# Optimization experiments

Hardware: AMD Instinct MI355X
Metric: run time of the kernel (lower is better)

The kernel has to match this reference:

```python
import jax, jax.numpy as jnp
import numpy as np

B, N0, NCLS = 8, 1024, 40
SPACING, SIGMA_FACTOR = 2.0, 1.0
BLOCKS = [[64, 64], [128, 128], [256, 1024]]
POOL_SIZES = [256, 64, 1]
FC1, FC2 = 512, 256
# 3x3x3 kernel translation grid (27-point support, hard-coded in ConvLayer)
GRID = jnp.asarray(np.array([[i, j, k] for i in (-1, 0, 1) for j in (-1, 0, 1) for k in (-1, 0, 1)], dtype=np.float32))  # [27,3]


def pcnn_conv(pc, feat, W, b, sigma):
    """Extension-operator point convolution.
    pc [B,N,3], feat [B,N,Cin], W [27,Cin,Cout], b [Cout].
    out[b,i,o] = relu( (1/N) * sum_l sum_j exp(-||p_i - p_j + t_l||^2/(2 ks^2)) f[b,j] @ W[l] + b )
    """
    ks = SIGMA_FACTOR * sigma
    trans = SPACING * sigma * GRID                      # [27,3]
    inv = 1.0 / (2.0 * ks * ks)
    diff = pc[:, :, None, :] - pc[:, None, :, :]        # [B,N,N,3]
    d2 = jnp.sum(diff * diff, -1)                       # [B,N,N]
    n = pc.shape[1]

    def body(acc, wt):
        t, Wl = wt                                      # t [3], Wl [Cin,Cout]
        # ||diff + t||^2 = d2 + 2 diff.t + |t|^2
        e = jnp.exp(-(d2 + 2.0 * jnp.einsum('bijd,d->bij', diff, t) + jnp.dot(t, t)) * inv)
        s = jnp.einsum('bij,bjc->bic', e, feat)         # Gaussian-weighted gather
        return acc + jnp.einsum('bic,co->bio', s, Wl), None

    out0 = jnp.zeros((pc.shape[0], n, W.shape[2]), feat.dtype)
    out, _ = jax.lax.scan(body, out0, (trans, W))
    return jax.nn.relu(out / n + b)


def fps(pts, m):
    """Farthest point sampling. pts [N,3] -> indices [m]."""
    d = jnp.sum((pts - pts[0]) ** 2, -1)
    idxs = jnp.zeros((m,), jnp.int32)

    def body(i, state):
        idxs, d = state
        nxt = jnp.argmax(d).astype(jnp.int32)
        idxs = idxs.at[i].set(nxt)
        d = jnp.minimum(d, jnp.sum((pts - pts[nxt]) ** 2, -1))
        return idxs, d

    idxs, _ = jax.lax.fori_loop(1, m, body, (idxs, d))
    return idxs


def pool(pc, feat, m):
    """FPS subsample to m centers, max-pool features over nearest-center clusters."""
    idx = jax.vmap(lambda p: fps(p, m))(pc)                      # [B,m]
    centers = jnp.take_along_axis(pc, idx[..., None], axis=1)    # [B,m,3]
    dist = jnp.sum((pc[:, :, None, :] - centers[:, None, :, :]) ** 2, -1)  # [B,N,m]
    assign = jnp.argmin(dist, -1)                                # [B,N]
    pooled = jax.vmap(lambda f, a: jax.ops.segment_max(f, a, num_segments=m))(feat, assign)
    return centers, pooled


def bn(x, g, b):
    mu = jnp.mean(x, 0)
    v = jnp.var(x, 0)
    return g * (x - mu) * jax.lax.rsqrt(v + 1e-5) + b


def setup_inputs() -> dict:
    key = jax.random.key(0)
    ks = jax.random.split(key, 24)
    inp = {"pc": jax.random.normal(ks[0], (B, 3, N0), jnp.float32)}
    chans = [4, 64, 64, 128, 128, 256, 1024]
    for i, (ci, co) in enumerate(zip(chans[:-1], chans[1:])):
        inp[f"w_c{i}"] = jax.random.normal(ks[1 + i], (27, ci, co), jnp.float32) * 0.05
        inp[f"b_c{i}"] = jnp.zeros((co,), jnp.float32)
    inp["w_fc1"] = jax.random.normal(ks[10], (1024, FC1), jnp.float32) * 0.03
    inp["g_fc1"] = jnp.ones((FC1,), jnp.float32)
    inp["be_fc1"] = jnp.zeros((FC1,), jnp.float32)
    inp["w_fc2"] = jax.random.normal(ks[11], (FC1, FC2), jnp.float32) * 0.05
    inp["g_fc2"] = jnp.ones((FC2,), jnp.float32)
    inp["be_fc2"] = jnp.zeros((FC2,), jnp.float32)
    inp["w_fc3"] = jax.random.normal(ks[12], (FC2, NCLS), jnp.float32) * 0.05
    inp["b_fc3"] = jnp.zeros((NCLS,), jnp.float32)
    return inp


def reference(pc, w_c0, b_c0, w_c1, b_c1, w_c2, b_c2, w_c3, b_c3, w_c4, b_c4, w_c5, b_c5,
              w_fc1, g_fc1, be_fc1, w_fc2, g_fc2, be_fc2, w_fc3, b_fc3):
    pts = jnp.transpose(pc, (0, 2, 1))                           # [B,N,3]
    b_, n0, _ = pts.shape
    feat = jnp.concatenate([pts, jnp.ones((b_, n0, 1), pts.dtype)], -1)  # [B,N,4]
    sigma = 1.0 / float(np.sqrt(n0))  # faithfully uses initial N for all blocks
    ws = [(w_c0, b_c0), (w_c1, b_c1), (w_c2, b_c2), (w_c3, b_c3), (w_c4, b_c4), (w_c5, b_c5)]
    idx = 0
    cur = pts
    for bi, block in enumerate(BLOCKS):
        for _ in block:
            W, bb = ws[idx]
            feat = pcnn_conv(cur, feat, W, bb, sigma)
            idx += 1
        cur, feat = pool(cur, feat, POOL_SIZES[bi])
    x = feat.reshape(b_, -1)                                     # [B,1024]
    x = jax.nn.relu(bn(x @ w_fc1, g_fc1, be_fc1))
    x = jax.nn.relu(bn(x @ w_fc2, g_fc2, be_fc2))
    return x @ w_fc3 + b_fc3
```

## Files before the change

### kernel.cpp

```cpp
#include <hip/hip_runtime.h>
#include <cstdint>
#include <cstddef>
#include <cmath>

constexpr int B = 8;
constexpr int N0 = 1024;
constexpr int CAP = 64;
using u16 = unsigned short;

typedef __bf16 bf16x8 __attribute__((ext_vector_type(8)));
typedef float f32x4 __attribute__((ext_vector_type(4)));

__device__ inline u16 f2bf(float x) {
  unsigned u = __float_as_uint(x);
  return (u16)((u + 0x7fffu + ((u >> 16) & 1u)) >> 16);
}
__device__ inline float bf2f(u16 h) { return __uint_as_float(((unsigned)h) << 16); }
__device__ inline int swk2(int row, int k) {
  int s = (((row >> 2) ^ (row >> 4)) & 3);
  return ((((k >> 3) ^ s) << 3) | (k & 7));
}

__global__ __launch_bounds__(256) void k_prep(const float* __restrict__ pc,
                                              float* __restrict__ pts,
                                              float* __restrict__ feat0,
                                              uint4* __restrict__ p3, int n3,
                                              uint4* __restrict__ p6, int n6,
                                              uint4* __restrict__ p9, int n9) {
  int idx = blockIdx.x * blockDim.x + threadIdx.x;
  if (idx < B * N0) {
    int b = idx / N0, i = idx - b * N0;
    float x = pc[(b * 3 + 0) * N0 + i];
    float y = pc[(b * 3 + 1) * N0 + i];
    float z = pc[(b * 3 + 2) * N0 + i];
    pts[idx * 3 + 0] = x; pts[idx * 3 + 1] = y; pts[idx * 3 + 2] = z;
    feat0[idx * 4 + 0] = x; feat0[idx * 4 + 1] = y; feat0[idx * 4 + 2] = z; feat0[idx * 4 + 3] = 1.0f;
  }
  uint4 v = make_uint4(0xFFFFFFFFu, 0xFFFFFFFFu, 0xFFFFFFFFu, 0xFFFFFFFFu);
  for (int i = idx; i < n3; i += B * N0) p3[i] = v;
  for (int i = idx; i < n6; i += B * N0) p6[i] = v;
  for (int i = idx; i < n9; i += B * N0) p9[i] = v;
}

__global__ __launch_bounds__(256) void k_pairs(const float* __restrict__ pts,
                                               int* __restrict__ pidx, int* __restrict__ pcnt,
                                               int N) {
  const int r = blockIdx.x * 4 + (threadIdx.x >> 6);
  const int lane = threadIdx.x & 63;
  const int b = r / N;
  const float px = pts[(size_t)r * 3 + 0];
  const float py = pts[(size_t)r * 3 + 1];
  const float pz = pts[(size_t)r * 3 + 2];
  int* row = pidx + (size_t)r * CAP;
  int base = 0;
  for (int j0 = 0; j0 < N; j0 += 64) {
    int j = j0 + lane;
    float dx = px - pts[((size_t)b * N + j) * 3 + 0];
    float dy = py - pts[((size_t)b * N + j) * 3 + 1];
    float dz = pz - pts[((size_t)b * N + j) * 3 + 2];
    float d2 = dx * dx + dy * dy + dz * dz;
    bool keep = d2 <= 0.1228f;
    unsigned long long mk = __ballot(keep);
    int pos = __popcll(mk & ((1ull << lane) - 1ull));
    if (keep) { int s = base + pos; if (s < CAP) row[s] = j; }
    base += __popcll(mk);
  }
  if (lane == 0) pcnt[r] = base < CAP ? base : CAP;
}

__device__ __forceinline__ void econ_dev(float (*eL)[28],
                                         const float* __restrict__ pts,
                                         const float* __restrict__ feat,
                                         const int* __restrict__ pidx,
                                         const int* __restrict__ pcnt,
                                         u16* __restrict__ Shi, u16* __restrict__ Slo,
                                         int N, int Cin, int K, int Kpad, int mbase,
                                         int blockX) {
  const int g = mbase + blockX;
  const int b = g / N;
  const int t = threadIdx.x;
  const int w = t >> 6, lane = t & 63;
  const bool cact = t < Cin;
  const float px = pts[(size_t)g * 3 + 0];
  const float py = pts[(size_t)g * 3 + 1];
  const float pz = pts[(size_t)g * 3 + 2];
  float sxc = 0.f, syc = 0.f, szc = 0.f, cst = 0.f;
  if (lane < 27) {
    int a = lane / 9, bb = (lane / 3) % 3, cc = lane % 3;
    sxc = (a == 0) ? 64.f : ((a == 2) ? -64.f : 0.f);
    syc = (bb == 0) ? 64.f : ((bb == 2) ? -64.f : 0.f);
    szc = (cc == 0) ? 64.f : ((cc == 2) ? -64.f : 0.f);
    cst = -2.f * (float)((a != 1) + (bb != 1) + (cc != 1));
  }
  float acc[27];
#pragma unroll
  for (int l = 0; l < 27; ++l) acc[l] = 0.f;
  const int n = pcnt[g];
  const int* row = pidx + (size_t)g * CAP;
  for (int p = 0; p < n; ++p) {
    int j = row[p];
    size_t jb = (size_t)b * N + j;
    float dx = px - pts[jb * 3 + 0];
    float dy = py - pts[jb * 3 + 1];
    float dz = pz - pts[jb * 3 + 2];
    float d2 = dx * dx + dy * dy + dz * dz;
    if (lane < 27) {
      float ex = fmaf(-512.f, d2, fmaf(sxc, dx, fmaf(syc, dy, fmaf(szc, dz, cst))));
      eL[w][lane] = __expf(ex);
    }
    asm volatile("s_waitcnt lgkmcnt(0)" ::: "memory");
    __builtin_amdgcn_sched_barrier(0);
    float fv = cact ? feat[jb * Cin + t] : 0.f;
#pragma unroll
    for (int l = 0; l < 27; ++l) acc[l] = fmaf(eL[w][l], fv, acc[l]);
  }
  size_t rowo = (size_t)blockX * Kpad;
  if (cact) {
#pragma unroll
    for (int l = 0; l < 27; ++l) {
      float v = acc[l];
      u16 h = f2bf(v);
      u16 lo = f2bf(v - bf2f(h));
      Shi[rowo + (size_t)l * Cin + t] = h;
      Slo[rowo + (size_t)l * Cin + t] = lo;
    }
  }
  if (Kpad > K && t >= Cin && t < Cin + (Kpad - K)) {
    size_t po = rowo + K + (t - Cin);
    Shi[po] = 0; Slo[po] = 0;
  }
}

__global__ void k_econtract(const float* __restrict__ pts, const float* __restrict__ feat,
                            const int* __restrict__ pidx, const int* __restrict__ pcnt,
                            u16* __restrict__ Shi, u16* __restrict__ Slo,
                            int N, int Cin, int K, int Kpad, int mbase) {
  __shared__ float eL[4][28];
  econ_dev(eL, pts, feat, pidx, pcnt, Shi, Slo, N, Cin, K, Kpad, mbase, blockIdx.x);
}

template <int CTRL>
__device__ __forceinline__ float dppmaxf(float v) {
  int o = __builtin_amdgcn_update_dpp(0, __float_as_int(v), CTRL, 0xF, 0xF, true);
  return fmaxf(v, __int_as_float(o));
}
__device__ __forceinline__ float wavemaxf(float v) {
  v = dppmaxf<0xB1>(v);
  v = dppmaxf<0x4E>(v);
  v = dppmaxf<0x141>(v);
  v = dppmaxf<0x140>(v);
  v = dppmaxf<0x142>(v);
  v = dppmaxf<0x143>(v);
  return __uint_as_float((unsigned)__builtin_amdgcn_readlane(__float_as_int(v), 63));
}

#define FPS_LOAD(i) \
  float qx##i = src[3 * i + 0], qy##i = src[3 * i + 1], qz##i = src[3 * i + 2];
#define FPS_PIN(i) \
  asm volatile("" : "+v"(qx##i), "+v"(qy##i), "+v"(qz##i));
#define FPS_D0(i) \
  float d##i; { float ax = __fsub_rn(qx##i, x0), ay = __fsub_rn(qy##i, y0), az = __fsub_rn(qz##i, z0); \
    d##i = __fadd_rn(__fadd_rn(__fmul_rn(ax, ax), __fmul_rn(ay, ay)), __fmul_rn(az, az)); }
#define FPS_UPD(i) \
  { float ax = __fsub_rn(qx##i, cx), ay = __fsub_rn(qy##i, cy), az = __fsub_rn(qz##i, cz); \
    float nd = __fadd_rn(__fadd_rn(__fmul_rn(ax, ax), __fmul_rn(ay, ay)), __fmul_rn(az, az)); \
    d##i = fminf(d##i, nd); }
#define FPS_SEL(i) \
  { bool e = (d##i == lbest); sx = e ? qx##i : sx; sy = e ? qy##i : sy; sz = e ? qz##i : sz; }

__device__ __noinline__ void fps1024_dev(const float* __restrict__ P,
                                         float* __restrict__ centers, int m, int b, int t) {
  const float* src = P + t * 16 * 3;
  FPS_LOAD(0) FPS_LOAD(1) FPS_LOAD(2) FPS_LOAD(3)
  FPS_LOAD(4) FPS_LOAD(5) FPS_LOAD(6) FPS_LOAD(7)
  FPS_LOAD(8) FPS_LOAD(9) FPS_LOAD(10) FPS_LOAD(11)
  FPS_LOAD(12) FPS_LOAD(13) FPS_LOAD(14) FPS_LOAD(15)
  FPS_PIN(0) FPS_PIN(1) FPS_PIN(2) FPS_PIN(3)
  FPS_PIN(4) FPS_PIN(5) FPS_PIN(6) FPS_PIN(7)
  FPS_PIN(8) FPS_PIN(9) FPS_PIN(10) FPS_PIN(11)
  FPS_PIN(12) FPS_PIN(13) FPS_PIN(14) FPS_PIN(15)
  float x0 = P[0], y0 = P[1], z0 = P[2];
  FPS_D0(0) FPS_D0(1) FPS_D0(2) FPS_D0(3)
  FPS_D0(4) FPS_D0(5) FPS_D0(6) FPS_D0(7)
  FPS_D0(8) FPS_D0(9) FPS_D0(10) FPS_D0(11)
  FPS_D0(12) FPS_D0(13) FPS_D0(14) FPS_D0(15)
  if (t == 0) {
    centers[(size_t)b * m * 3 + 0] = x0;
    centers[(size_t)b * m * 3 + 1] = y0;
    centers[(size_t)b * m * 3 + 2] = z0;
  }
  for (int it = 1; it < m; ++it) {
    float lbest;
    {
      float a0 = fmaxf(d0, d1), a1 = fmaxf(d2, d3), a2 = fmaxf(d4, d5), a3 = fmaxf(d6, d7);
      float a4 = fmaxf(d8, d9), a5 = fmaxf(d10, d11), a6 = fmaxf(d12, d13), a7 = fmaxf(d14, d15);
      float b0 = fmaxf(a0, a1), b1 = fmaxf(a2, a3), b2 = fmaxf(a4, a5), b3 = fmaxf(a6, a7);
      lbest = fmaxf(fmaxf(b0, b1), fmaxf(b2, b3));
    }
    float sx = qx15, sy = qy15, sz = qz15;
    FPS_SEL(14) FPS_SEL(13) FPS_SEL(12) FPS_SEL(11)
    FPS_SEL(10) FPS_SEL(9) FPS_SEL(8) FPS_SEL(7)
    FPS_SEL(6) FPS_SEL(5) FPS_SEL(4) FPS_SEL(3)
    FPS_SEL(2) FPS_SEL(1) FPS_SEL(0)
    float wmax = wavemaxf(lbest);
    unsigned long long mask = __ballot(lbest == wmax);
    int fl = __ffsll((long long)mask) - 1;
    float cx = __uint_as_float((unsigned)__builtin_amdgcn_readlane(__float_as_int(sx), fl));
    float cy = __uint_as_float((unsigned)__builtin_amdgcn_readlane(__float_as_int(sy), fl));
    float cz = __uint_as_float((unsigned)__builtin_amdgcn_readlane(__float_as_int(sz), fl));
    if (t == 0) {
      centers[((size_t)b * m + it) * 3 + 0] = cx;
      centers[((size_t)b * m + it) * 3 + 1] = cy;
      centers[((size_t)b * m + it) * 3 + 2] = cz;
    }
    FPS_UPD(0) FPS_UPD(1) FPS_UPD(2) FPS_UPD(3)
    FPS_UPD(4) FPS_UPD(5) FPS_UPD(6) FPS_UPD(7)
    FPS_UPD(8) FPS_UPD(9) FPS_UPD(10) FPS_UPD(11)
    FPS_UPD(12) FPS_UPD(13) FPS_UPD(14) FPS_UPD(15)
  }
}

__device__ __noinline__ void fps256_dev(const float* __restrict__ P,
                                        float* __restrict__ centers, int m, int b, int t) {
  const float* src = P + t * 4 * 3;
  FPS_LOAD(0) FPS_LOAD(1) FPS_LOAD(2) FPS_LOAD(3)
  FPS_PIN(0) FPS_PIN(1) FPS_PIN(2) FPS_PIN(3)
  float x0 = P[0], y0 = P[1], z0 = P[2];
  FPS_D0(0) FPS_D0(1) FPS_D0(2) FPS_D0(3)
  if (t == 0) {
    centers[(size_t)b * m * 3 + 0] = x0;
    centers[(size_t)b * m * 3 + 1] = y0;
    centers[(size_t)b * m * 3 + 2] = z0;
  }
  for (int it = 1; it < m; ++it) {
    float lbest = fmaxf(fmaxf(d0, d1), fmaxf(d2, d3));
    float sx = qx3, sy = qy3, sz = qz3;
    FPS_SEL(2) FPS_SEL(1) FPS_SEL(0)
    float wmax = wavemaxf(lbest);
    unsigned long long mask = __ballot(lbest == wmax);
    int fl = __ffsll((long long)mask) - 1;
    float cx = __uint_as_float((unsigned)__builtin_amdgcn_readlane(__float_as_int(sx), fl));
    float cy = __uint_as_float((unsigned)__builtin_amdgcn_readlane(__float_as_int(sy), fl));
    float cz = __uint_as_float((unsigned)__builtin_amdgcn_readlane(__float_as_int(sz), fl));
    if (t == 0) {
      centers[((size_t)b * m + it) * 3 + 0] = cx;
      centers[((size_t)b * m + it) * 3 + 1] = cy;
      centers[((size_t)b * m + it) * 3 + 2] = cz;
    }
    FPS_UPD(0) FPS_UPD(1) FPS_UPD(2) FPS_UPD(3)
  }
}

__global__ __launch_bounds__(64, 1) void k_econtract_fps(
    const float* __restrict__ pts, const float* __restrict__ feat,
    const int* __restrict__ pidx, const int* __restrict__ pcnt,
    u16* __restrict__ Shi, u16* __restrict__ Slo,
    int N, int Cin, int K, int Kpad, int mbase,
    int fpsMode, const float* __restrict__ fpsPts, float* __restrict__ fpsCenters, int fpsM) {
  __shared__ float eL[4][28];
  const int nEcon = gridDim.x - B;
  if ((int)blockIdx.x >= nEcon) {
    const int b = blockIdx.x - nEcon;
    const int t = threadIdx.x;
    if (fpsMode == 1) fps1024_dev(fpsPts + (size_t)b * 1024 * 3, fpsCenters, fpsM, b, t);
    else fps256_dev(fpsPts + (size_t)b * 256 * 3, fpsCenters, fpsM, b, t);
    return;
  }
  econ_dev(eL, pts, feat, pidx, pcnt, Shi, Slo, N, Cin, K, Kpad, mbase, blockIdx.x);
}

__global__ __launch_bounds__(512) void k_gemm_mfma(const u16* __restrict__ Shi,
                                                   const u16* __restrict__ Slo,
                                                   const float* __restrict__ W,
                                                   const float* __restrict__ bias,
                                                   float* __restrict__ out,
                                                   float* __restrict__ P,
                                                   int K, int Kpad, int Cout, float scale,
                                                   int mcur) {
  __shared__ u16 As[2][2][32][40];
  __shared__ u16 Bs[2][2][64][40];
  __shared__ float xch[4][64][8];
  const int t = threadIdx.x;
  const int h = t >> 8;
  const int tl = t & 255;
  const int nb = blockIdx.x * 64;
  const int m0 = blockIdx.y * 32;
  const int l = t & 63, w = t >> 6;
  const int ks = w >> 2, wq = w & 3;
  const int wm = (wq >> 1) * 16, wn = (wq & 1) * 32;
  const int la = l & 15, lg = l >> 4;
  const int ntiles = Kpad >> 6;
  const int KZ = gridDim.z, z = blockIdx.z;
  const int q = ntiles / KZ, r = ntiles % KZ;
  const int t0 = z * q + (z < r ? z : r);
  const int cnt = q + (z < r ? 1 : 0);
  const int ar = tl >> 3, ak = (tl & 7) * 4;
  const size_t aOff = (size_t)(m0 + ar) * Kpad + h * 32 + ak;
  const int aw = swk2(ar, ak);
  const int kp = (tl >> 4) * 2, n4 = (tl & 15) * 4;
  f32x4 acc0 = {0.f, 0.f, 0.f, 0.f}, acc1 = {0.f, 0.f, 0.f, 0.f};

  for (int kt = 0; kt < cnt; ++kt) {
    const int k0 = (t0 + kt) * 64;
    *(ushort4*)&As[h][0][ar][aw] = *(const ushort4*)(Shi + aOff + k0);
    *(ushort4*)&As[h][1][ar][aw] = *(const ushort4*)(Slo + aOff + k0);
    {
      int gk0 = k0 + h * 32 + kp;
      float4 b0 = make_float4(0.f, 0.f, 0.f, 0.f), b1 = b0;
      if (gk0 < K) b0 = *(const float4*)(W + (size_t)gk0 * Cout + nb + n4);
      if (gk0 + 1 < K) b1 = *(const float4*)(W + (size_t)(gk0 + 1) * Cout + nb + n4);
      float v0[4] = {b0.x, b0.y, b0.z, b0.w};
      float v1[4] = {b1.x, b1.y, b1.z, b1.w};
#pragma unroll
      for (int e = 0; e < 4; ++e) {
        int n = n4 + e;
        int kw = swk2(n, kp);
        u16 h0 = f2bf(v0[e]);
        u16 l0 = f2bf(v0[e] - bf2f(h0));
        u16 h1 = f2bf(v1[e]);
        u16 l1 = f2bf(v1[e] - bf2f(h1));
        *(unsigned*)&Bs[h][0][n][kw] = (unsigned)h0 | ((unsigned)h1 << 16);
        *(unsigned*)&Bs[h][1][n][kw] = (unsigned)l0 | ((unsigned)l1 << 16);
      }
    }
    __syncthreads();
    bf16x8 ah = *(const bf16x8*)&As[ks][0][wm + la][swk2(wm + la, lg * 8)];
    bf16x8 al = *(const bf16x8*)&As[ks][1][wm + la][swk2(wm + la, lg * 8)];
    bf16x8 bh0 = *(const bf16x8*)&Bs[ks][0][wn + la][swk2(wn + la, lg * 8)];
    bf16x8 bl0 = *(const bf16x8*)&Bs[ks][1][wn + la][swk2(wn + la, lg * 8)];
    bf16x8 bh1 = *(const bf16x8*)&Bs[ks][0][wn + 16 + la][swk2(wn + 16 + la, lg * 8)];
    bf16x8 bl1 = *(const bf16x8*)&Bs[ks][1][wn + 16 + la][swk2(wn + 16 + la, lg * 8)];
    acc0 = __builtin_amdgcn_mfma_f32_16x16x32_bf16(ah, bh0, acc0, 0, 0, 0);
    acc1 = __builtin_amdgcn_mfma_f32_16x16x32_bf16(ah, bh1, acc1, 0, 0, 0);
    acc0 = __builtin_amdgcn_mfma_f32_16x16x32_bf16(al, bh0, acc0, 0, 0, 0);
    acc1 = __builtin_amdgcn_mfma_f32_16x16x32_bf16(al, bh1, acc1, 0, 0, 0);
    acc0 = __builtin_amdgcn_mfma_f32_16x16x32_bf16(ah, bl0, acc0, 0, 0, 0);
    acc1 = __builtin_amdgcn_mfma_f32_16x16x32_bf16(ah, bl1, acc1, 0, 0, 0);
    __syncthreads();
  }
  if (w >= 4) {
#pragma unroll
    for (int r2 = 0; r2 < 4; ++r2) { xch[wq][l][r2] = acc0[r2]; xch[wq][l][r2 + 4] = acc1[r2]; }
  }
  __syncthreads();
  if (w < 4) {
#pragma unroll
    for (int r2 = 0; r2 < 4; ++r2) { acc0[r2] += xch[wq][l][r2]; acc1[r2] += xch[wq][l][r2 + 4]; }
    if (gridDim.z == 1) {
#pragma unroll
      for (int r2 = 0; r2 < 4; ++r2) {
        int gm = m0 + wm + lg * 4 + r2;
        int gn0 = nb + wn + la;
        out[(size_t)gm * Cout + gn0] = fmaxf(fmaf(acc0[r2], scale, bias[gn0]), 0.f);
        int gn1 = gn0 + 16;
        out[(size_t)gm * Cout + gn1] = fmaxf(fmaf(acc1[r2], scale, bias[gn1]), 0.f);
      }
    } else {
      float* Pz = P + (size_t)z * mcur * Cout;
#pragma unroll
      for (int r2 = 0; r2 < 4; ++r2) {
        int gm = m0 + wm + lg * 4 + r2;
        int gn0 = nb + wn + la;
        Pz[(size_t)gm * Cout + gn0] = acc0[r2];
        Pz[(size_t)gm * Cout + gn0 + 16] = acc1[r2];
      }
    }
  }
}

__global__ __launch_bounds__(256) void k_reduce(const float* __restrict__ P,
                                                const float* __restrict__ bias,
                                                float* __restrict__ out,
                                                int n4, int Cout, int KZ, float scale,
                                                int stride) {
  int i = blockIdx.x * 256 + threadIdx.x;
  if (i >= n4) return;
  float4 s = *(const float4*)(P + (size_t)i * 4);
  for (int z = 1; z < KZ; ++z) {
    float4 v = *(const float4*)(P + (size_t)z * stride + (size_t)i * 4);
    s.x += v.x; s.y += v.y; s.z += v.z; s.w += v.w;
  }
  int c = (i * 4) % Cout;
  float4 bb = *(const float4*)(bias + c);
  float4 o;
  o.x = fmaxf(fmaf(s.x, scale, bb.x), 0.f);
  o.y = fmaxf(fmaf(s.y, scale, bb.y), 0.f);
  o.z = fmaxf(fmaf(s.z, scale, bb.z), 0.f);
  o.w = fmaxf(fmaf(s.w, scale, bb.w), 0.f);
  *(float4*)(out + (size_t)i * 4) = o;
}

__global__ __launch_bounds__(64) void k_center0(const float* __restrict__ pts,
                                                float* __restrict__ centers,
                                                int* __restrict__ assign) {
  const int b = blockIdx.x, t = threadIdx.x;
  if (t < 3) centers[b * 3 + t] = pts[(size_t)b * 64 * 3 + t];
  assign[b * 64 + t] = 0;
}

__global__ __launch_bounds__(256) void k_assign(const float* __restrict__ pts,
                                                const float* __restrict__ centers,
                                                int* __restrict__ assign, int N, int m) {
  __shared__ float cs[256 * 3];
  const int t = threadIdx.x;
  const int idx = blockIdx.x * 256 + t;
  const int b = (blockIdx.x * 256) / N;
  for (int i = t; i < m * 3; i += 256) cs[i] = centers[(size_t)b * m * 3 + i];
  __syncthreads();
  float px = pts[(size_t)idx * 3 + 0], py = pts[(size_t)idx * 3 + 1], pz = pts[(size_t)idx * 3 + 2];
  float best = 3.4e38f; int bk = 0;
  for (int k = 0; k < m; ++k) {
    float dx = __fsub_rn(px, cs[k * 3 + 0]);
    float dy = __fsub_rn(py, cs[k * 3 + 1]);
    float dz = __fsub_rn(pz, cs[k * 3 + 2]);
    float dd = __fadd_rn(__fadd_rn(__fmul_rn(dx, dx), __fmul_rn(dy, dy)), __fmul_rn(dz, dz));
    if (dd < best) { best = dd; bk = k; }
  }
  assign[idx] = bk;
}

__global__ __launch_bounds__(256) void k_segmax(const float* __restrict__ feat,
                                                const int* __restrict__ assign,
                                                float* __restrict__ pooled,
                                                int N, int m, int C) {
  int idx = blockIdx.x * blockDim.x + threadIdx.x;
  if (idx >= B * N * C) return;
  int b = idx / (N * C);
  int r = idx - b * N * C;
  int i = r / C;
  int c = r - i * C;
  int a = assign[b * N + i];
  atomicMax((int*)&pooled[((size_t)b * m + a) * C + c], __float_as_int(feat[idx]));
}

template <int K, int COUT, bool BNR>
__global__ __launch_bounds__(256) void k_fc(const float* __restrict__ x,
                                            const float* __restrict__ w,
                                            const float* __restrict__ g,
                                            const float* __restrict__ be,
                                            float* __restrict__ out) {
  __shared__ float ys[8][33];
  int t = threadIdx.x;
  int n = t >> 5, cl = t & 31;
  int c = blockIdx.x * 32 + cl;
  float acc = 0.f;
  if (c < COUT) {
    const float* xr = x + n * K;
    float a0 = 0.f, a1 = 0.f, a2 = 0.f, a3 = 0.f;
    for (int k = 0; k < K; k += 4) {
      a0 = fmaf(xr[k + 0], w[(size_t)(k + 0) * COUT + c], a0);
      a1 = fmaf(xr[k + 1], w[(size_t)(k + 1) * COUT + c], a1);
      a2 = fmaf(xr[k + 2], w[(size_t)(k + 2) * COUT + c], a2);
      a3 = fmaf(xr[k + 3], w[(size_t)(k + 3) * COUT + c], a3);
    }
    acc = (a0 + a1) + (a2 + a3);
  }
  ys[n][cl] = acc;
  __syncthreads();
  if (c >= COUT) return;
  if (BNR) {
    float mu = 0.f;
#pragma unroll
    for (int q = 0; q < 8; ++q) mu += ys[q][cl];
    mu *= 0.125f;
    float var = 0.f;
#pragma unroll
    for (int q = 0; q < 8; ++q) { float dv = ys[q][cl] - mu; var = fmaf(dv, dv, var); }
    var *= 0.125f;
    float rs = 1.f / sqrtf(var + 1e-5f);
    float v = g[c] * (acc - mu) * rs + be[c];
    out[n * COUT + c] = fmaxf(v, 0.f);
  } else {
    out[n * COUT + c] = acc + be[c];
  }
}

extern "C" void kernel_launch(void* const* d_in, const int* in_sizes, int n_in,
                              void* d_out, int out_size, void* d_ws, size_t ws_size,
                              hipStream_t stream) {
  (void)in_sizes; (void)n_in; (void)out_size;
  const float* pc = (const float*)d_in[0];
  const float* Wc[6]; const float* bc[6];
  for (int l = 0; l < 6; ++l) { Wc[l] = (const float*)d_in[1 + 2 * l]; bc[l] = (const float*)d_in[2 + 2 * l]; }
  const float* w1 = (const float*)d_in[13];
  const float* g1 = (const float*)d_in[14];
  const float* be1 = (const float*)d_in[15];
  const float* w2 = (const float*)d_in[16];
  const float* g2 = (const float*)d_in[17];
  const float* be2 = (const float*)d_in[18];
  const float* w3 = (const float*)d_in[19];
  const float* b3 = (const float*)d_in[20];

  float* ws = (float*)d_ws;
  size_t o = 0;
  auto A = [&](size_t n) { size_t r = o; o += (n + 63) & ~(size_t)63; return r; };
  const size_t PTS0 = A((size_t)B * 1024 * 3);
  const size_t PTS1 = A((size_t)B * 256 * 3);
  const size_t PTS2 = A((size_t)B * 64 * 3);
  const size_t PTS3 = A((size_t)B * 3);
  const size_t F0  = A((size_t)B * 1024 * 4);
  const size_t FB1 = A((size_t)B * 1024 * 64);
  const size_t FB2 = A((size_t)B * 1024 * 64);
  const size_t FB3 = A((size_t)B * 256 * 64);
  const size_t FB4 = A((size_t)B * 256 * 128);
  const size_t FB5 = A((size_t)B * 256 * 128);
  const size_t FB6 = A((size_t)B * 64 * 128);
  const size_t FB7 = A((size_t)B * 64 * 256);
  const size_t FB8 = A((size_t)B * 64 * 1024);
  const size_t FB9 = A((size_t)B * 1024);
  const size_t ASSIGN = A((size_t)B * 1024);
  const size_t Y1 = A((size_t)8 * 512);
  const size_t Y2 = A((size_t)8 * 256);
  const size_t PIDX = A((size_t)B * 1024 * CAP);
  const size_t PCNT = A((size_t)B * 1024);
  const size_t dynB = o * sizeof(float);

  int* pidx = (int*)(ws + PIDX);
  int* pcnt = (int*)(ws + PCNT);

  k_prep<<<dim3((B * N0 + 255) / 256), dim3(256), 0, stream>>>(
      pc, ws + PTS0, ws + F0,
      (uint4*)(ws + FB3), B * 256 * 64 / 4,
      (uint4*)(ws + FB6), B * 64 * 128 / 4,
      (uint4*)(ws + FB9), B * 1024 / 4);

  auto conv = [&](size_t ptsOff, size_t finOff, size_t foutOff, int Npts, int Cin, int Cout,
                  const float* W, const float* bias,
                  int fpsMode, size_t fpsPtsOff, size_t fpsCtrOff, int fpsM) {
    const int M = B * Npts;
    const int K = 27 * Cin;
    const int Kpad = (K + 63) & ~63;
    const size_t availB = (ws_size > dynB) ? ws_size - dynB : 0;
    size_t pResB = availB / 4;
    if (pResB > (size_t)13 << 20) pResB = (size_t)13 << 20;
    const size_t sByte = availB - pResB;
    long mc = (long)(sByte / ((size_t)Kpad * 4)) & ~31L;
    int Mc = (int)((mc < (long)M) ? mc : (long)M);
    if (Mc < 32) Mc = 32;
    u16* Shi = (u16*)((char*)d_ws + dynB);
    u16* Slo = Shi + (size_t)Mc * Kpad;
    float* P = (float*)(Shi + (size_t)2 * Mc * Kpad);
    const int mch = (M + Mc - 1) / Mc;
    const float scale = 1.f / (float)Npts;
    const int blk = (Cin <= 64) ? 64 : Cin;
    const int ntiles = Kpad >> 6;
    for (int mcb = 0; mcb < mch; ++mcb) {
      const int mb0 = mcb * Mc;
      const int mcur = ((M - mb0) < Mc) ? (M - mb0) : Mc;
      if (mcb == 0 && fpsMode && blk == 64) {
        k_econtract_fps<<<dim3(mcur + B), dim3(64), 0, stream>>>(
            ws + ptsOff, ws + finOff, pidx, pcnt, Shi, Slo, Npts, Cin, K, Kpad, mb0,
            fpsMode, ws + fpsPtsOff, ws + fpsCtrOff, fpsM);
      } else {
        k_econtract<<<dim3(mcur), dim3(blk), 0, stream>>>(ws + ptsOff, ws + finOff, pidx, pcnt,
                                                          Shi, Slo, Npts, Cin, K, Kpad, mb0);
      }
      const int gx = Cout / 64, gy = mcur / 32;
      int kz = 1024 / (gx * gy);
      if (kz < 1) kz = 1;
      if (kz > ntiles) kz = ntiles;
      if (kz > 16) kz = 16;
      long pcap = (long)(pResB / ((size_t)mcur * Cout * 4));
      if ((long)kz > pcap) kz = (pcap < 1) ? 1 : (int)pcap;
      float* outp = ws + foutOff + (size_t)mb0 * Cout;
      k_gemm_mfma<<<dim3(gx, gy, kz), dim3(512), 0, stream>>>(
          Shi, Slo, W, bias, outp, P, K, Kpad, Cout, scale, mcur);
      if (kz > 1) {
        int n4 = mcur * Cout / 4;
        k_reduce<<<dim3((n4 + 255) / 256), dim3(256), 0, stream>>>(
            P, bias, outp, n4, Cout, kz, scale, mcur * Cout);
      }
    }
  };

  k_pairs<<<dim3(B * 1024 / 4), dim3(256), 0, stream>>>(ws + PTS0, pidx, pcnt, 1024);
  conv(PTS0, F0, FB1, 1024, 4, 64, Wc[0], bc[0], 0, 0, 0, 0);
  conv(PTS0, FB1, FB2, 1024, 64, 64, Wc[1], bc[1], 1, PTS0, PTS1, 256);
  k_assign<<<dim3(B * 1024 / 256), dim3(256), 0, stream>>>(ws + PTS0, ws + PTS1, (int*)(ws + ASSIGN), 1024, 256);
  k_segmax<<<dim3((B * 1024 * 64 + 255) / 256), dim3(256), 0, stream>>>(ws + FB2, (int*)(ws + ASSIGN), ws + FB3, 1024, 256, 64);
  k_pairs<<<dim3(B * 256 / 4), dim3(256), 0, stream>>>(ws + PTS1, pidx, pcnt, 256);
  conv(PTS1, FB3, FB4, 256, 64, 128, Wc[2], bc[2], 2, PTS1, PTS2, 64);
  conv(PTS1, FB4, FB5, 256, 128, 128, Wc[3], bc[3], 0, 0, 0, 0);
  k_assign<<<dim3(B * 256 / 256), dim3(256), 0, stream>>>(ws + PTS1, ws + PTS2, (int*)(ws + ASSIGN), 256, 64);
  k_segmax<<<dim3((B * 256 * 128 + 255) / 256), dim3(256), 0, stream>>>(ws + FB5, (int*)(ws + ASSIGN), ws + FB6, 256, 64, 128);
  k_pairs<<<dim3(B * 64 / 4), dim3(256), 0, stream>>>(ws + PTS2, pidx, pcnt, 64);
  conv(PTS2, FB6, FB7, 64, 128, 256, Wc[4], bc[4], 0, 0, 0, 0);
  conv(PTS2, FB7, FB8, 64, 256, 1024, Wc[5], bc[5], 0, 0, 0, 0);
  k_center0<<<dim3(B), dim3(64), 0, stream>>>(ws + PTS2, ws + PTS3, (int*)(ws + ASSIGN));
  k_segmax<<<dim3((B * 64 * 1024 + 255) / 256), dim3(256), 0, stream>>>(ws + FB8, (int*)(ws + ASSIGN), ws + FB9, 64, 1, 1024);
  k_fc<1024, 512, true><<<dim3(512 / 32), dim3(256), 0, stream>>>(ws + FB9, w1, g1, be1, ws + Y1);
  k_fc<512, 256, true><<<dim3(256 / 32), dim3(256), 0, stream>>>(ws + Y1, w2, g2, be2, ws + Y2);
  k_fc<256, 40, false><<<dim3(2), dim3(256), 0, stream>>>(ws + Y2, w3, nullptr, b3, (float*)d_out);
}
```

Before: 426.9 us.

## Split FPS iterations across econtract and GEMM kernels of multiple convs

Farthest point sampling is made resumable: each call runs a range of iterations and saves its per-point min-distance state to a workspace buffer. The FPS work for each pool is then spread over the econtract and GEMM launches of several conv layers as extra blocks, including conv0 which is independent of FPS. The goal is to hide the serial FPS latency behind parallel conv work instead of leaving it on the critical path of one launch. In exchange it adds global state round-trips, extra grid rows in the GEMM, and a dependency on launch ordering.

```diff
diff --git a/kernel.cpp b/kernel.cpp
--- a/kernel.cpp
+++ b/kernel.cpp
@@ -158,8 +158,8 @@
   float qx##i = src[3 * i + 0], qy##i = src[3 * i + 1], qz##i = src[3 * i + 2];
 #define FPS_PIN(i) \
   asm volatile("" : "+v"(qx##i), "+v"(qy##i), "+v"(qz##i));
-#define FPS_D0(i) \
-  float d##i; { float ax = __fsub_rn(qx##i, x0), ay = __fsub_rn(qy##i, y0), az = __fsub_rn(qz##i, z0); \
+#define FPS_D0A(i) \
+  { float ax = __fsub_rn(qx##i, x0), ay = __fsub_rn(qy##i, y0), az = __fsub_rn(qz##i, z0); \
     d##i = __fadd_rn(__fadd_rn(__fmul_rn(ax, ax), __fmul_rn(ay, ay)), __fmul_rn(az, az)); }
 #define FPS_UPD(i) \
   { float ax = __fsub_rn(qx##i, cx), ay = __fsub_rn(qy##i, cy), az = __fsub_rn(qz##i, cz); \
@@ -169,8 +169,9 @@
   { bool e = (d##i == lbest); sx = e ? qx##i : sx; sy = e ? qy##i : sy; sz = e ? qz##i : sz; }
 
 __device__ __noinline__ void fps1024_dev(const float* __restrict__ P,
-                                         float* __restrict__ centers, int m, int b, int t) {
-  const float* src = P + t * 16 * 3;
+                                         float* __restrict__ centers, int m, int b, int t,
+                                         int it0, int it1, float* __restrict__ Dst) {
+  const float* src = P + t * 48;
   FPS_LOAD(0) FPS_LOAD(1) FPS_LOAD(2) FPS_LOAD(3)
   FPS_LOAD(4) FPS_LOAD(5) FPS_LOAD(6) FPS_LOAD(7)
   FPS_LOAD(8) FPS_LOAD(9) FPS_LOAD(10) FPS_LOAD(11)
@@ -179,17 +180,26 @@
   FPS_PIN(4) FPS_PIN(5) FPS_PIN(6) FPS_PIN(7)
   FPS_PIN(8) FPS_PIN(9) FPS_PIN(10) FPS_PIN(11)
   FPS_PIN(12) FPS_PIN(13) FPS_PIN(14) FPS_PIN(15)
-  float x0 = P[0], y0 = P[1], z0 = P[2];
-  FPS_D0(0) FPS_D0(1) FPS_D0(2) FPS_D0(3)
-  FPS_D0(4) FPS_D0(5) FPS_D0(6) FPS_D0(7)
-  FPS_D0(8) FPS_D0(9) FPS_D0(10) FPS_D0(11)
-  FPS_D0(12) FPS_D0(13) FPS_D0(14) FPS_D0(15)
-  if (t == 0) {
-    centers[(size_t)b * m * 3 + 0] = x0;
-    centers[(size_t)b * m * 3 + 1] = y0;
-    centers[(size_t)b * m * 3 + 2] = z0;
-  }
-  for (int it = 1; it < m; ++it) {
+  float d0, d1, d2, d3, d4, d5, d6, d7, d8, d9, d10, d11, d12, d13, d14, d15;
+  if (it0 == 1) {
+    float x0 = P[0], y0 = P[1], z0 = P[2];
+    FPS_D0A(0) FPS_D0A(1) FPS_D0A(2) FPS_D0A(3)
+    FPS_D0A(4) FPS_D0A(5) FPS_D0A(6) FPS_D0A(7)
+    FPS_D0A(8) FPS_D0A(9) FPS_D0A(10) FPS_D0A(11)
+    FPS_D0A(12) FPS_D0A(13) FPS_D0A(14) FPS_D0A(15)
+    if (t == 0) {
+      centers[(size_t)b * m * 3 + 0] = x0;
+      centers[(size_t)b * m * 3 + 1] = y0;
+      centers[(size_t)b * m * 3 + 2] = z0;
+    }
+  } else {
+    const float* ds = Dst + t * 16;
+    d0 = ds[0]; d1 = ds[1]; d2 = ds[2]; d3 = ds[3];
+    d4 = ds[4]; d5 = ds[5]; d6 = ds[6]; d7 = ds[7];
+    d8 = ds[8]; d9 = ds[9]; d10 = ds[10]; d11 = ds[11];
+    d12 = ds[12]; d13 = ds[13]; d14 = ds[14]; d15 = ds[15];
+  }
+  for (int it = it0; it < it1; ++it) {
     float lbest;
     {
       float a0 = fmaxf(d0, d1), a1 = fmaxf(d2, d3), a2 = fmaxf(d4, d5), a3 = fmaxf(d6, d7);
@@ -218,21 +228,35 @@
     FPS_UPD(8) FPS_UPD(9) FPS_UPD(10) FPS_UPD(11)
     FPS_UPD(12) FPS_UPD(13) FPS_UPD(14) FPS_UPD(15)
   }
+  if (it1 < m) {
+    float* ds = Dst + t * 16;
+    ds[0] = d0; ds[1] = d1; ds[2] = d2; ds[3] = d3;
+    ds[4] = d4; ds[5] = d5; ds[6] = d6; ds[7] = d7;
+    ds[8] = d8; ds[9] = d9; ds[10] = d10; ds[11] = d11;
+    ds[12] = d12; ds[13] = d13; ds[14] = d14; ds[15] = d15;
+  }
 }
 
 __device__ __noinline__ void fps256_dev(const float* __restrict__ P,
-                                        float* __restrict__ centers, int m, int b, int t) {
-  const float* src = P + t * 4 * 3;
+                                        float* __restrict__ centers, int m, int b, int t,
+                                        int it0, int it1, float* __restrict__ Dst) {
+  const float* src = P + t * 12;
   FPS_LOAD(0) FPS_LOAD(1) FPS_LOAD(2) FPS_LOAD(3)
   FPS_PIN(0) FPS_PIN(1) FPS_PIN(2) FPS_PIN(3)
-  float x0 = P[0], y0 = P[1], z0 = P[2];
-  FPS_D0(0) FPS_D0(1) FPS_D0(2) FPS_D0(3)
-  if (t == 0) {
-    centers[(size_t)b * m * 3 + 0] = x0;
-    centers[(size_t)b * m * 3 + 1] = y0;
-    centers[(size_t)b * m * 3 + 2] = z0;
-  }
-  for (int it = 1; it < m; ++it) {
+  float d0, d1, d2, d3;
+  if (it0 == 1) {
+    float x0 = P[0], y0 = P[1], z0 = P[2];
+    FPS_D0A(0) FPS_D0A(1) FPS_D0A(2) FPS_D0A(3)
+    if (t == 0) {
+      centers[(size_t)b * m * 3 + 0] = x0;
+      centers[(size_t)b * m * 3 + 1] = y0;
+      centers[(size_t)b * m * 3 + 2] = z0;
+    }
+  } else {
+    const float* ds = Dst + t * 4;
+    d0 = ds[0]; d1 = ds[1]; d2 = ds[2]; d3 = ds[3];
+  }
+  for (int it = it0; it < it1; ++it) {
     float lbest = fmaxf(fmaxf(d0, d1), fmaxf(d2, d3));
     float sx = qx3, sy = qy3, sz = qz3;
     FPS_SEL(2) FPS_SEL(1) FPS_SEL(0)
@@ -249,6 +273,10 @@
     }
     FPS_UPD(0) FPS_UPD(1) FPS_UPD(2) FPS_UPD(3)
   }
+  if (it1 < m) {
+    float* ds = Dst + t * 4;
+    ds[0] = d0; ds[1] = d1; ds[2] = d2; ds[3] = d3;
+  }
 }
 
 __global__ __launch_bounds__(64, 1) void k_econtract_fps(
@@ -256,14 +284,17 @@
     const int* __restrict__ pidx, const int* __restrict__ pcnt,
     u16* __restrict__ Shi, u16* __restrict__ Slo,
     int N, int Cin, int K, int Kpad, int mbase,
-    int fpsMode, const float* __restrict__ fpsPts, float* __restrict__ fpsCenters, int fpsM) {
+    int fpsMode, const float* __restrict__ fpsPts, float* __restrict__ fpsCenters, int fpsM,
+    int it0, int it1, float* __restrict__ fpsD) {
   __shared__ float eL[4][28];
   const int nEcon = gridDim.x - B;
   if ((int)blockIdx.x >= nEcon) {
     const int b = blockIdx.x - nEcon;
     const int t = threadIdx.x;
-    if (fpsMode == 1) fps1024_dev(fpsPts + (size_t)b * 1024 * 3, fpsCenters, fpsM, b, t);
-    else fps256_dev(fpsPts + (size_t)b * 256 * 3, fpsCenters, fpsM, b, t);
+    if (fpsMode == 1) fps1024_dev(fpsPts + (size_t)b * 1024 * 3, fpsCenters, fpsM, b, t,
+                                  it0, it1, fpsD + (size_t)b * 1024);
+    else fps256_dev(fpsPts + (size_t)b * 256 * 3, fpsCenters, fpsM, b, t,
+                    it0, it1, fpsD + (size_t)b * 256);
     return;
   }
   econ_dev(eL, pts, feat, pidx, pcnt, Shi, Slo, N, Cin, K, Kpad, mbase, blockIdx.x);
@@ -276,7 +307,21 @@
                                                    float* __restrict__ out,
                                                    float* __restrict__ P,
                                                    int K, int Kpad, int Cout, float scale,
-                                                   int mcur) {
+                                                   int mcur, int gyReal,
+                                                   int fpsMode, const float* __restrict__ fpsPts,
+                                                   float* __restrict__ fpsCenters, int fpsM,
+                                                   int it0, int it1, float* __restrict__ fpsD) {
+  if ((int)blockIdx.y >= gyReal) {
+    if (blockIdx.z == 0 && fpsMode && threadIdx.x < 64) {
+      const int b = blockIdx.y - gyReal;
+      const int t = threadIdx.x;
+      if (fpsMode == 1) fps1024_dev(fpsPts + (size_t)b * 1024 * 3, fpsCenters, fpsM, b, t,
+                                    it0, it1, fpsD + (size_t)b * 1024);
+      else fps256_dev(fpsPts + (size_t)b * 256 * 3, fpsCenters, fpsM, b, t,
+                      it0, it1, fpsD + (size_t)b * 256);
+    }
+    return;
+  }
   __shared__ u16 As[2][2][32][40];
   __shared__ u16 Bs[2][2][64][40];
   __shared__ float xch[4][64][8];
@@ -511,6 +556,7 @@
   const size_t ASSIGN = A((size_t)B * 1024);
   const size_t Y1 = A((size_t)8 * 512);
   const size_t Y2 = A((size_t)8 * 256);
+  const size_t FPSD = A((size_t)B * 1024);
   const size_t PIDX = A((size_t)B * 1024 * CAP);
   const size_t PCNT = A((size_t)B * 1024);
   const size_t dynB = o * sizeof(float);
@@ -526,7 +572,8 @@
 
   auto conv = [&](size_t ptsOff, size_t finOff, size_t foutOff, int Npts, int Cin, int Cout,
                   const float* W, const float* bias,
-                  int fpsMode, size_t fpsPtsOff, size_t fpsCtrOff, int fpsM) {
+                  int fpsMode, size_t fpsPtsOff, size_t fpsCtrOff, int fpsM,
+                  int eIt0, int eIt1, int gIt0, int gIt1) {
     const int M = B * Npts;
     const int K = 27 * Cin;
     const int Kpad = (K + 63) & ~63;
@@ -547,10 +594,11 @@
     for (int mcb = 0; mcb < mch; ++mcb) {
       const int mb0 = mcb * Mc;
       const int mcur = ((M - mb0) < Mc) ? (M - mb0) : Mc;
-      if (mcb == 0 && fpsMode && blk == 64) {
+      const bool host = (mcb == 0 && fpsMode != 0);
+      if (host && blk == 64) {
         k_econtract_fps<<<dim3(mcur + B), dim3(64), 0, stream>>>(
             ws + ptsOff, ws + finOff, pidx, pcnt, Shi, Slo, Npts, Cin, K, Kpad, mb0,
-            fpsMode, ws + fpsPtsOff, ws + fpsCtrOff, fpsM);
+            fpsMode, ws + fpsPtsOff, ws + fpsCtrOff, fpsM, eIt0, eIt1, ws + FPSD);
       } else {
         k_econtract<<<dim3(mcur), dim3(blk), 0, stream>>>(ws + ptsOff, ws + finOff, pidx, pcnt,
                                                           Shi, Slo, Npts, Cin, K, Kpad, mb0);
@@ -563,8 +611,10 @@
       long pcap = (long)(pResB / ((size_t)mcur * Cout * 4));
       if ((long)kz > pcap) kz = (pcap < 1) ? 1 : (int)pcap;
       float* outp = ws + foutOff + (size_t)mb0 * Cout;
-      k_gemm_mfma<<<dim3(gx, gy, kz), dim3(512), 0, stream>>>(
-          Shi, Slo, W, bias, outp, P, K, Kpad, Cout, scale, mcur);
+      const int gyE = host ? B : 0;
+      k_gemm_mfma<<<dim3(gx, gy + gyE, kz), dim3(512), 0, stream>>>(
+          Shi, Slo, W, bias, outp, P, K, Kpad, Cout, scale, mcur, gy,
+          host ? fpsMode : 0, ws + fpsPtsOff, ws + fpsCtrOff, fpsM, gIt0, gIt1, ws + FPSD);
       if (kz > 1) {
         int n4 = mcur * Cout / 4;
         k_reduce<<<dim3((n4 + 255) / 256), dim3(256), 0, stream>>>(
@@ -574,18 +624,18 @@
   };
 
   k_pairs<<<dim3(B * 1024 / 4), dim3(256), 0, stream>>>(ws + PTS0, pidx, pcnt, 1024);
-  conv(PTS0, F0, FB1, 1024, 4, 64, Wc[0], bc[0], 0, 0, 0, 0);
-  conv(PTS0, FB1, FB2, 1024, 64, 64, Wc[1], bc[1], 1, PTS0, PTS1, 256);
+  conv(PTS0, F0, FB1, 1024, 4, 64, Wc[0], bc[0], 1, PTS0, PTS1, 256, 1, 65, 65, 129);
+  conv(PTS0, FB1, FB2, 1024, 64, 64, Wc[1], bc[1], 1, PTS0, PTS1, 256, 129, 193, 193, 256);
   k_assign<<<dim3(B * 1024 / 256), dim3(256), 0, stream>>>(ws + PTS0, ws + PTS1, (int*)(ws + ASSIGN), 1024, 256);
   k_segmax<<<dim3((B * 1024 * 64 + 255) / 256), dim3(256), 0, stream>>>(ws + FB2, (int*)(ws + ASSIGN), ws + FB3, 1024, 256, 64);
   k_pairs<<<dim3(B * 256 / 4), dim3(256), 0, stream>>>(ws + PTS1, pidx, pcnt, 256);
-  conv(PTS1, FB3, FB4, 256, 64, 128, Wc[2], bc[2], 2, PTS1, PTS2, 64);
-  conv(PTS1, FB4, FB5, 256, 128, 128, Wc[3], bc[3], 0, 0, 0, 0);
+  conv(PTS1, FB3, FB4, 256, 64, 128, Wc[2], bc[2], 2, PTS1, PTS2, 64, 1, 33, 33, 64);
+  conv(PTS1, FB4, FB5, 256, 128, 128, Wc[3], bc[3], 0, 0, 0, 0, 0, 0, 0, 0);
   k_assign<<<dim3(B * 256 / 256), dim3(256), 0, stream>>>(ws + PTS1, ws + PTS2, (int*)(ws + ASSIGN), 256, 64);
   k_segmax<<<dim3((B * 256 * 128 + 255) / 256), dim3(256), 0, stream>>>(ws + FB5, (int*)(ws + ASSIGN), ws + FB6, 256, 64, 128);
   k_pairs<<<dim3(B * 64 / 4), dim3(256), 0, stream>>>(ws + PTS2, pidx, pcnt, 64);
-  conv(PTS2, FB6, FB7, 64, 128, 256, Wc[4], bc[4], 0, 0, 0, 0);
-  conv(PTS2, FB7, FB8, 64, 256, 1024, Wc[5], bc[5], 0, 0, 0, 0);
+  conv(PTS2, FB6, FB7, 64, 128, 256, Wc[4], bc[4], 0, 0, 0, 0, 0, 0, 0, 0);
+  conv(PTS2, FB7, FB8, 64, 256, 1024, Wc[5], bc[5], 0, 0, 0, 0, 0, 0, 0, 0);
   k_center0<<<dim3(B), dim3(64), 0, stream>>>(ws + PTS2, ws + PTS3, (int*)(ws + ASSIGN));
   k_segmax<<<dim3((B * 64 * 1024 + 255) / 256), dim3(256), 0, stream>>>(ws + FB8, (int*)(ws + ASSIGN), ws + FB9, 64, 1, 1024);
   k_fc<1024, 512, true><<<dim3(512 / 32), dim3(256), 0, stream>>>(ws + FB9, w1, g1, be1, ws + Y1);
```

After: 564.5 us. +32.2%, slower.
